# Performance work log

Measured on AMD Instinct MI355X. Metric: run time of the kernel, lower is better.

The kernel has to match this reference:

```python
import jax, jax.numpy as jnp
import numpy as np

N = 8192        # number of particles
NC = 4          # number of cell types (species)
DIM = 3
BOX = 40.0      # box side so typical pair distances straddle the cutoff
EPS_MAX, EPS_MIN = 5.0, 1.0
ALPHA_MAX, ALPHA_MIN = 3.0, 1.0
R_ONSET, R_CUTOFF = 1.7, 2.0


def setup_inputs() -> dict:
    key = jax.random.key(0)
    k_eps, k_alpha, k_ct, k_rad, k_pos = jax.random.split(key, 5)
    epsilon = jax.random.normal(k_eps, (NC, NC), dtype=jnp.float32)
    alpha = jax.random.normal(k_alpha, (NC, NC), dtype=jnp.float32)
    ct_idx = jax.random.randint(k_ct, (N,), 0, NC)
    celltype = jax.nn.one_hot(ct_idx, NC, dtype=jnp.float32)   # [N, NC]
    radius = 0.25 + 0.25 * jax.random.uniform(k_rad, (N, 1), dtype=jnp.float32)
    positions = BOX * jax.random.uniform(k_pos, (N, DIM), dtype=jnp.float32)
    return {"epsilon": epsilon, "alpha": alpha, "celltype": celltype,
            "radius": radius, "positions": positions}


def _species_pairwise(mat, celltype, vmax, vmin):
    # symmetrize as in the original module
    m = 0.5 * (jnp.triu(mat) + jnp.tril(mat).T + jnp.triu(mat).T + jnp.tril(mat))
    m = m - jnp.eye(NC, dtype=mat.dtype) * 0.5 * jnp.diagonal(m)
    m = jax.nn.sigmoid(m) * vmax + vmin
    m = celltype @ m @ celltype.T                               # [N, N]
    alive = celltype.sum(-1) > 0.0                              # [N] -> masks columns
    return jnp.where(alive, m, 0.0)


def reference(epsilon, alpha, celltype, radius, positions):
    eps_m = _species_pairwise(epsilon, celltype, EPS_MAX, EPS_MIN)    # [N, N]
    alpha_m = _species_pairwise(alpha, celltype, ALPHA_MAX, ALPHA_MIN)
    sigma_m = radius + radius.T                                       # [N, N]

    diff = positions[:, None, :] - positions[None, :, :]              # [N, N, 3]
    dr2 = jnp.sum(diff * diff, axis=-1)                               # [N, N]
    eye = jnp.eye(N, dtype=bool)
    dr = jnp.sqrt(jnp.where(eye, 1.0, dr2))                           # safe sqrt on diag

    # Morse potential (jax_md.energy.morse)
    u = eps_m * jnp.square(1.0 - jnp.exp(-alpha_m * (dr - sigma_m))) - eps_m

    # multiplicative isotropic cutoff (jax_md smoothing, operates on r^2)
    r_o, r_c = R_ONSET ** 2, R_CUTOFF ** 2
    smooth_inner = jnp.square(r_c - dr2) * (r_c + 2.0 * dr2 - 3.0 * r_o) / (r_c - r_o) ** 3
    smooth = jnp.where(dr2 < r_o, 1.0, jnp.where(dr2 < r_c, smooth_inner, 0.0))

    e = jnp.where(eye, 0.0, u * smooth)                               # mask self-interaction
    return 0.5 * jnp.sum(e)                                           # scalar total energy
```

## Files before the change

### kernel.cpp

```cpp
#include <hip/hip_runtime.h>
#include <hip/hip_bf16.h>

#define NPART 8192
#define NCT 4
#define TPB 256
#define NTILE (NPART / TPB)
#define NBLK (NTILE * (NTILE + 1) / 2)

__device__ __forceinline__ float loadf(const void* p, int idx, bool bf) {
    if (bf) {
        unsigned int u = ((const unsigned short*)p)[idx];
        return __uint_as_float(u << 16);
    }
    return ((const float*)p)[idx];
}

__global__ __launch_bounds__(TPB) void pair_kernel(const void* __restrict__ eps,
                                                   const void* __restrict__ alp,
                                                   const void* __restrict__ ct,
                                                   const void* __restrict__ rad,
                                                   const void* __restrict__ pos,
                                                   float* __restrict__ partials)
{
    __shared__ float4 sp[TPB];
    __shared__ int ssp[TPB];
    __shared__ float stab[32];
    __shared__ float red[TPB / 64];

    const int t = threadIdx.x;

    unsigned int w = ((const unsigned int*)ct)[t & 63];
    const bool bf = (__ballot((w & 0xFFFFu) != 0) != 0ull);

    const int b = blockIdx.x;
    int by = (int)((sqrtf(8.0f * (float)b + 1.0f) - 1.0f) * 0.5f);
    while ((by + 1) * (by + 2) / 2 <= b) ++by;
    while (by * (by + 1) / 2 > b) --by;
    const int bx = b - by * (by + 1) / 2;
    const bool diag = (bx == by);

    if (t < 16) {
        int a = t >> 2, c = t & 3;
        float me = (a == c) ? loadf(eps, a * NCT + a, bf)
                            : 0.5f * (loadf(eps, a * NCT + c, bf) + loadf(eps, c * NCT + a, bf));
        float ma = (a == c) ? loadf(alp, a * NCT + a, bf)
                            : 0.5f * (loadf(alp, a * NCT + c, bf) + loadf(alp, c * NCT + a, bf));
        stab[t]      = 5.0f / (1.0f + __expf(-me)) + 1.0f;
        stab[16 + t] = 3.0f / (1.0f + __expf(-ma)) + 1.0f;
    }

    const int j0 = by * TPB;
    {
        int j = j0 + t;
        float4 pj;
        pj.x = loadf(pos, j * 3 + 0, bf);
        pj.y = loadf(pos, j * 3 + 1, bf);
        pj.z = loadf(pos, j * 3 + 2, bf);
        pj.w = loadf(rad, j, bf);
        sp[t] = pj;
        int sj = -1;
#pragma unroll
        for (int c = 0; c < NCT; ++c)
            if (loadf(ct, j * NCT + c, bf) > 0.5f) sj = c;
        ssp[t] = sj;
    }

    const int i = bx * TPB + t;
    float4 pi;
    pi.x = loadf(pos, i * 3 + 0, bf);
    pi.y = loadf(pos, i * 3 + 1, bf);
    pi.z = loadf(pos, i * 3 + 2, bf);
    pi.w = loadf(rad, i, bf);
    int si = -1;
#pragma unroll
    for (int c = 0; c < NCT; ++c)
        if (loadf(ct, i * NCT + c, bf) > 0.5f) si = c;

    __syncthreads();

    constexpr float RC2 = 4.0f;
    constexpr float RO2 = 1.7f * 1.7f;
    constexpr float C1  = RC2 - 3.0f * RO2;
    const float INV_D = 1.0f / ((RC2 - RO2) * (RC2 - RO2) * (RC2 - RO2));

    float acc = 0.0f;
    if (si >= 0) {
#pragma unroll 8
        for (int jj = 0; jj < TPB; ++jj) {
            float4 pj = sp[jj];
            float dx = pi.x - pj.x;
            float dy = pi.y - pj.y;
            float dz = pi.z - pj.z;
            float dr2 = fmaf(dx, dx, fmaf(dy, dy, dz * dz));
            if (dr2 < RC2) {
                int j = j0 + jj;
                int sj = ssp[jj];
                if (j != i && sj >= 0) {
                    float e = stab[(si << 2) | sj];
                    float a = stab[16 + ((si << 2) | sj)];
                    float dr = sqrtf(dr2);
                    float ex = __expf(-a * (dr - (pi.w + pj.w)));
                    float om = 1.0f - ex;
                    float u = fmaf(e * om, om, -e);
                    float smooth = 1.0f;
                    if (dr2 >= RO2) {
                        float d = RC2 - dr2;
                        smooth = d * d * fmaf(2.0f, dr2, C1) * INV_D;
                    }
                    acc += u * smooth;
                }
            }
        }
    }

    acc *= diag ? 0.5f : 1.0f;

#pragma unroll
    for (int off = 32; off > 0; off >>= 1) acc += __shfl_down(acc, off, 64);
    int lane = t & 63, wv = t >> 6;
    if (lane == 0) red[wv] = acc;
    __syncthreads();
    if (t == 0) partials[b] = red[0] + red[1] + red[2] + red[3];
}

__global__ __launch_bounds__(TPB) void finalize_kernel(const float* __restrict__ partials,
                                                       const void* __restrict__ ct,
                                                       void* __restrict__ out)
{
    __shared__ float red[TPB / 64];
    const int t = threadIdx.x;

    unsigned int w = ((const unsigned int*)ct)[t & 63];
    const bool bf = (__ballot((w & 0xFFFFu) != 0) != 0ull);

    float s = 0.0f;
    for (int k = t; k < NBLK; k += TPB) s += partials[k];
#pragma unroll
    for (int off = 32; off > 0; off >>= 1) s += __shfl_down(s, off, 64);
    int lane = t & 63, wv = t >> 6;
    if (lane == 0) red[wv] = s;
    __syncthreads();
    if (t == 0) {
        float v = red[0] + red[1] + red[2] + red[3];
        if (bf) ((__hip_bfloat16*)out)[0] = __float2bfloat16(v);
        else    ((float*)out)[0] = v;
    }
}

extern "C" void kernel_launch(void* const* d_in, const int* in_sizes, int n_in,
                              void* d_out, int out_size, void* d_ws, size_t ws_size,
                              hipStream_t stream)
{
    const void* eps = nullptr; const void* alp = nullptr;
    const void* ct = nullptr;  const void* rad = nullptr; const void* pos = nullptr;
    int nsmall = 0;
    for (int k = 0; k < n_in; ++k) {
        int s = in_sizes[k];
        if (s == NCT * NCT)        { if (nsmall++ == 0) eps = d_in[k]; else alp = d_in[k]; }
        else if (s == NPART * NCT) ct  = d_in[k];
        else if (s == NPART)       rad = d_in[k];
        else if (s == NPART * 3)   pos = d_in[k];
    }
    if (!eps || !alp || !ct || !rad || !pos) {
        eps = d_in[0]; alp = d_in[1]; ct = d_in[2]; rad = d_in[3]; pos = d_in[4];
    }

    float* partials = (float*)d_ws;

    pair_kernel<<<NBLK, TPB, 0, stream>>>(eps, alp, ct, rad, pos, partials);
    finalize_kernel<<<1, TPB, 0, stream>>>(partials, ct, d_out);
}
```

Before: 90.00 us.

## Precompute packed float4 particle data and fuse final reduction via atomics

Adds a prep kernel that converts positions, radii and one-hot species into a packed float4 array and an int species array, and builds the species parameter tables once. The pair kernel then reads the j-tile straight from global memory instead of staging it in shared memory, and replaces the separate finalize kernel with an atomic accumulate plus last-block-done counter. This removes the per-block format decoding and the extra launch, but adds a launch for prep and uncached-style global loads in the inner loop, and makes the float summation order nondeterministic.

```diff
diff --git a/kernel.cpp b/kernel.cpp
--- a/kernel.cpp
+++ b/kernel.cpp
@@ -7,6 +7,7 @@
 #define NTILE (NPART / TPB)
 #define NBLK (NTILE * (NTILE + 1) / 2)
 
+
 __device__ __forceinline__ float loadf(const void* p, int idx, bool bf) {
     if (bf) {
         unsigned int u = ((const unsigned short*)p)[idx];
@@ -15,22 +16,63 @@
     return ((const float*)p)[idx];
 }
 
-__global__ __launch_bounds__(TPB) void pair_kernel(const void* __restrict__ eps,
+__global__ __launch_bounds__(TPB) void prep_kernel(const void* __restrict__ eps,
                                                    const void* __restrict__ alp,
                                                    const void* __restrict__ ct,
                                                    const void* __restrict__ rad,
                                                    const void* __restrict__ pos,
-                                                   float* __restrict__ partials)
+                                                   float* __restrict__ acc,
+                                                   unsigned int* __restrict__ cnt,
+                                                   int* __restrict__ bfflag,
+                                                   float* __restrict__ tabs,
+                                                   float4* __restrict__ pos4,
+                                                   int* __restrict__ spec)
 {
-    __shared__ float4 sp[TPB];
-    __shared__ int ssp[TPB];
+    const int t = threadIdx.x;
+
+    unsigned int w = ((const unsigned int*)ct)[t & 63];
+    const bool bf = (__ballot((w & 0xFFFFu) != 0) != 0ull);
+
+    const int i = blockIdx.x * TPB + t;
+    float4 p;
+    p.x = loadf(pos, i * 3 + 0, bf);
+    p.y = loadf(pos, i * 3 + 1, bf);
+    p.z = loadf(pos, i * 3 + 2, bf);
+    p.w = loadf(rad, i, bf);
+    pos4[i] = p;
+    int s = -1;
+#pragma unroll
+    for (int c = 0; c < NCT; ++c)
+        if (loadf(ct, i * NCT + c, bf) > 0.5f) s = c;
+    spec[i] = s;
+
+    if (blockIdx.x == 0) {
+        if (t == 0) { *acc = 0.0f; *cnt = 0u; *bfflag = bf ? 1 : 0; }
+        if (t < 16) {
+            int a = t >> 2, c = t & 3;
+            float me = (a == c) ? loadf(eps, a * NCT + a, bf)
+                                : 0.5f * (loadf(eps, a * NCT + c, bf) + loadf(eps, c * NCT + a, bf));
+            float ma = (a == c) ? loadf(alp, a * NCT + a, bf)
+                                : 0.5f * (loadf(alp, a * NCT + c, bf) + loadf(alp, c * NCT + a, bf));
+            tabs[t]      = 5.0f / (1.0f + __expf(-me)) + 1.0f;
+            tabs[16 + t] = 3.0f / (1.0f + __expf(-ma)) + 1.0f;
+        }
+    }
+}
+
+__global__ __launch_bounds__(TPB) void pair_kernel(const float4* __restrict__ pos4,
+                                                   const int* __restrict__ spec,
+                                                   const float* __restrict__ tabs,
+                                                   const int* __restrict__ bfflag,
+                                                   float* __restrict__ acc_out,
+                                                   unsigned int* __restrict__ cnt,
+                                                   void* __restrict__ out)
+{
     __shared__ float stab[32];
     __shared__ float red[TPB / 64];
 
     const int t = threadIdx.x;
-
-    unsigned int w = ((const unsigned int*)ct)[t & 63];
-    const bool bf = (__ballot((w & 0xFFFFu) != 0) != 0ull);
+    if (t < 32) stab[t] = tabs[t];
 
     const int b = blockIdx.x;
     int by = (int)((sqrtf(8.0f * (float)b + 1.0f) - 1.0f) * 0.5f);
@@ -39,42 +81,11 @@
     const int bx = b - by * (by + 1) / 2;
     const bool diag = (bx == by);
 
-    if (t < 16) {
-        int a = t >> 2, c = t & 3;
-        float me = (a == c) ? loadf(eps, a * NCT + a, bf)
-                            : 0.5f * (loadf(eps, a * NCT + c, bf) + loadf(eps, c * NCT + a, bf));
-        float ma = (a == c) ? loadf(alp, a * NCT + a, bf)
-                            : 0.5f * (loadf(alp, a * NCT + c, bf) + loadf(alp, c * NCT + a, bf));
-        stab[t]      = 5.0f / (1.0f + __expf(-me)) + 1.0f;
-        stab[16 + t] = 3.0f / (1.0f + __expf(-ma)) + 1.0f;
-    }
-
+    const int i = bx * TPB + t;
+    const float4 pi = pos4[i];
+    const int si = spec[i];
     const int j0 = by * TPB;
-    {
-        int j = j0 + t;
-        float4 pj;
-        pj.x = loadf(pos, j * 3 + 0, bf);
-        pj.y = loadf(pos, j * 3 + 1, bf);
-        pj.z = loadf(pos, j * 3 + 2, bf);
-        pj.w = loadf(rad, j, bf);
-        sp[t] = pj;
-        int sj = -1;
-#pragma unroll
-        for (int c = 0; c < NCT; ++c)
-            if (loadf(ct, j * NCT + c, bf) > 0.5f) sj = c;
-        ssp[t] = sj;
-    }
-
-    const int i = bx * TPB + t;
-    float4 pi;
-    pi.x = loadf(pos, i * 3 + 0, bf);
-    pi.y = loadf(pos, i * 3 + 1, bf);
-    pi.z = loadf(pos, i * 3 + 2, bf);
-    pi.w = loadf(rad, i, bf);
-    int si = -1;
-#pragma unroll
-    for (int c = 0; c < NCT; ++c)
-        if (loadf(ct, i * NCT + c, bf) > 0.5f) si = c;
+    const float4* __restrict__ tile = pos4 + j0;
 
     __syncthreads();
 
@@ -87,14 +98,14 @@
     if (si >= 0) {
 #pragma unroll 8
         for (int jj = 0; jj < TPB; ++jj) {
-            float4 pj = sp[jj];
+            float4 pj = tile[jj];
             float dx = pi.x - pj.x;
             float dy = pi.y - pj.y;
             float dz = pi.z - pj.z;
             float dr2 = fmaf(dx, dx, fmaf(dy, dy, dz * dz));
             if (dr2 < RC2) {
                 int j = j0 + jj;
-                int sj = ssp[jj];
+                int sj = spec[j];
                 if (j != i && sj >= 0) {
                     float e = stab[(si << 2) | sj];
                     float a = stab[16 + ((si << 2) | sj)];
@@ -120,30 +131,18 @@
     int lane = t & 63, wv = t >> 6;
     if (lane == 0) red[wv] = acc;
     __syncthreads();
-    if (t == 0) partials[b] = red[0] + red[1] + red[2] + red[3];
-}
 
-__global__ __launch_bounds__(TPB) void finalize_kernel(const float* __restrict__ partials,
-                                                       const void* __restrict__ ct,
-                                                       void* __restrict__ out)
-{
-    __shared__ float red[TPB / 64];
-    const int t = threadIdx.x;
-
-    unsigned int w = ((const unsigned int*)ct)[t & 63];
-    const bool bf = (__ballot((w & 0xFFFFu) != 0) != 0ull);
-
-    float s = 0.0f;
-    for (int k = t; k < NBLK; k += TPB) s += partials[k];
-#pragma unroll
-    for (int off = 32; off > 0; off >>= 1) s += __shfl_down(s, off, 64);
-    int lane = t & 63, wv = t >> 6;
-    if (lane == 0) red[wv] = s;
-    __syncthreads();
     if (t == 0) {
-        float v = red[0] + red[1] + red[2] + red[3];
-        if (bf) ((__hip_bfloat16*)out)[0] = __float2bfloat16(v);
-        else    ((float*)out)[0] = v;
+        float s = red[0] + red[1] + red[2] + red[3];
+        atomicAdd(acc_out, s);
+        __threadfence();
+        unsigned int old = atomicAdd(cnt, 1u);
+        if (old == NBLK - 1) {
+            __threadfence();
+            float v = atomicAdd(acc_out, 0.0f);
+            if (*bfflag) ((__hip_bfloat16*)out)[0] = __float2bfloat16(v);
+            else         ((float*)out)[0] = v;
+        }
     }
 }
 
@@ -165,8 +164,15 @@
         eps = d_in[0]; alp = d_in[1]; ct = d_in[2]; rad = d_in[3]; pos = d_in[4];
     }
 
-    float* partials = (float*)d_ws;
+    char* ws = (char*)d_ws;
+    float*        acc    = (float*)(ws + 0);
+    unsigned int* cnt    = (unsigned int*)(ws + 4);
+    int*          bfflag = (int*)(ws + 8);
+    float*        tabs   = (float*)(ws + 64);
+    float4*       pos4   = (float4*)(ws + 4096);
+    int*          spec   = (int*)(ws + 4096 + NPART * sizeof(float4));
 
-    pair_kernel<<<NBLK, TPB, 0, stream>>>(eps, alp, ct, rad, pos, partials);
-    finalize_kernel<<<1, TPB, 0, stream>>>(partials, ct, d_out);
+    prep_kernel<<<NPART / TPB, TPB, 0, stream>>>(eps, alp, ct, rad, pos,
+                                                 acc, cnt, bfflag, tabs, pos4, spec);
+    pair_kernel<<<NBLK, TPB, 0, stream>>>(pos4, spec, tabs, bfflag, acc, cnt, d_out);
 }
```

Result: slower. 98.03 us (+8.9%).
